# Kernel tuning notes

Measured on AMD Instinct MI355X. Metric: run time of the kernel, lower is better.

The kernel has to match this reference:

```python
import jax, jax.numpy as jnp
import numpy as np

B, C, H, W = 16, 1536, 32, 32
M = 64      # num_clusters
L = 128     # cluster_dim
G = 256     # token_dim
HID = 512
OT_ITERS = 3
EPS = 1e-6


def setup_inputs() -> dict:
    key = jax.random.key(0)
    ks = jax.random.split(key, 12)
    def w(k, shape, fan_in):
        return jax.random.normal(k, shape, jnp.float32) * (1.0 / np.sqrt(fan_in))
    return {
        'x': jax.random.normal(ks[0], (B, C, H, W), jnp.float32),
        't': jax.random.normal(ks[1], (B, C), jnp.float32),
        # token_features: Linear(C->512), ReLU, Linear(512->G)
        'Wt1': w(ks[2], (HID, C), C), 'bt1': jnp.zeros((HID,), jnp.float32),
        'Wt2': w(ks[3], (G, HID), HID), 'bt2': jnp.zeros((G,), jnp.float32),
        # cluster_features: 1x1 Conv(C->512), ReLU, 1x1 Conv(512->L)
        'Wc1': w(ks[4], (HID, C), C), 'bc1': jnp.zeros((HID,), jnp.float32),
        'Wc2': w(ks[5], (L, HID), HID), 'bc2': jnp.zeros((L,), jnp.float32),
        # score: 1x1 Conv(C->512), ReLU, 1x1 Conv(512->M)
        'Ws1': w(ks[6], (HID, C), C), 'bs1': jnp.zeros((HID,), jnp.float32),
        'Ws2': w(ks[7], (M, HID), HID), 'bs2': jnp.zeros((M,), jnp.float32),
        # temp_predictor: Conv1d(L->1, k=1)
        'Wtp': w(ks[8], (L,), L), 'btp': jnp.zeros((), jnp.float32),
        'dust_bin': jnp.asarray(1.0, jnp.float32),
        'burst_b': jnp.asarray(0.0, jnp.float32),
        'burst_p': jnp.asarray(1.0, jnp.float32),
        'lambda_discount': jnp.asarray(0.5, jnp.float32),
    }


def _log_optimal_transport(scores, alpha, iters):
    # scores: [B, m, n]; alpha: scalar dust-bin logit
    b, m, n = scores.shape
    Z0 = jnp.concatenate([scores, jnp.broadcast_to(alpha, (b, 1, n))], axis=1)  # [B, m+1, n]
    norm = -jnp.log(jnp.asarray(m + n, scores.dtype))
    log_mu = jnp.concatenate([jnp.full((m,), norm, scores.dtype),
                              (jnp.log(jnp.asarray(n, scores.dtype)) + norm)[None]])  # [m+1]
    log_nu = jnp.full((n,), norm, scores.dtype)
    u = jnp.zeros((b, m + 1), scores.dtype)
    v = jnp.zeros((b, n), scores.dtype)
    for _ in range(iters):
        u = log_mu - jax.nn.logsumexp(Z0 + v[:, None, :], axis=2)
        v = log_nu - jax.nn.logsumexp(Z0 + u[:, :, None], axis=1)
    return Z0 + u[:, :, None] + v[:, None, :] - norm


def _l2norm(a, axis):
    return a / jnp.maximum(jnp.linalg.norm(a, axis=axis, keepdims=True), 1e-12)


def _forward(x, t, Wt1, bt1, Wt2, bt2, Wc1, bc1, Wc2, bc2, Ws1, bs1, Ws2, bs2,
             Wtp, btp, dust_bin, burst_b, burst_p, lambda_discount):
    b, c, h, w = x.shape
    n = h * w
    xf = x.reshape(b, c, n)  # [B, C, N] (1x1 convs == per-pixel MLP)
    # cluster features f: [B, L, N]
    h1 = jax.nn.relu(jnp.einsum('bcn,oc->bon', xf, Wc1) + bc1[:, None])
    f = jnp.einsum('bhn,lh->bln', h1, Wc2) + bc2[:, None]
    # assignment scores p: [B, M, N]
    h2 = jax.nn.relu(jnp.einsum('bcn,oc->bon', xf, Ws1) + bs1[:, None])
    p = jnp.einsum('bhn,mh->bmn', h2, Ws2) + bs2[:, None]
    # global token: [B, G]
    tok = jax.nn.relu(t @ Wt1.T + bt1) @ Wt2.T + bt2
    # Sinkhorn OT soft assignment, drop dust bin row
    P = jnp.exp(_log_optimal_transport(p, dust_bin, OT_ITERS))[:, :-1, :]  # [B, M, N]
    # burst-aware weighting
    f_norm = _l2norm(f, axis=1)                                  # [B, L, N]
    T_i = jax.nn.softplus(jnp.einsum('bln,l->bn', f, Wtp) + btp)  # [B, N]
    sim = jnp.einsum('bli,blj->bij', f_norm, f_norm)              # [B, N, N]
    T_avg = (T_i[:, :, None] + T_i[:, None, :]) * 0.5
    burst_w = jax.nn.sigmoid(T_avg * sim + burst_b)
    discount = jnp.clip(jnp.sum(burst_w, axis=-1) ** burst_p, 1e-3, 1e3)  # [B, N]
    lam = jax.nn.sigmoid(lambda_discount)
    P_adj = (1.0 - lam) * P + lam * (P / (discount[:, None, :] + EPS))
    # local aggregation: (f[:, :, None, :] * P[:, None, :, :]).sum(-1) == batched matmul
    agg = jnp.einsum('bln,bmn->blm', f, P_adj)  # [B, L, M]
    agg = _l2norm(agg, axis=1).reshape(b, -1)   # [B, L*M]
    tok_n = _l2norm(tok, axis=-1)
    g = jnp.concatenate([tok_n, agg], axis=-1)  # [B, G + L*M]
    return _l2norm(g, axis=-1)


def reference(x, t, Wt1, bt1, Wt2, bt2, Wc1, bc1, Wc2, bc2, Ws1, bs1, Ws2, bs2,
              Wtp, btp, dust_bin, burst_b, burst_p, lambda_discount):
    return _forward(x, t, Wt1, bt1, Wt2, bt2, Wc1, bc1, Wc2, bc2, Ws1, bs1, Ws2, bs2,
                    Wtp, btp, dust_bin, burst_b, burst_p, lambda_discount)
```

## Files before the change

kernel.cpp:

```cpp
#include <hip/hip_runtime.h>
#include <math.h>

#define B_   16
#define C_   1536
#define N_   1024
#define M_   64
#define L_   128
#define G_   256
#define HID_ 512

typedef __attribute__((ext_vector_type(8))) short short8;
typedef __attribute__((ext_vector_type(4))) float floatx4;

__device__ __forceinline__ unsigned short f2bf_rne(float x) {
    unsigned u = __float_as_uint(x);
    unsigned r = u + 0x7fffu + ((u >> 16) & 1u);
    return (unsigned short)(r >> 16);
}
__device__ __forceinline__ unsigned pack_bf2(float lo, float hi) {
    unsigned a = __float_as_uint(lo) + 0x8000u;
    unsigned b = __float_as_uint(hi) + 0x8000u;
    return (a >> 16) | (b & 0xffff0000u);
}

__device__ __forceinline__ void gl2lds16(const void* g, void* l) {
    __builtin_amdgcn_global_load_lds(
        (const __attribute__((address_space(1))) void*)g,
        (__attribute__((address_space(3))) void*)l, 16, 0, 0);
}

__global__ __launch_bounds__(256) void cast_w_kernel(
    const float* __restrict__ Wc1, const float* __restrict__ Ws1,
    const float* __restrict__ Wc2, const float* __restrict__ Ws2,
    unsigned short* __restrict__ Wbf, unsigned short* __restrict__ W2)
{
    const int V1 = 393216;
    const int VH = 196608;
    int idx = blockIdx.x * 256 + threadIdx.x;
    if (idx < V1) {
        const float4* src = (idx < VH) ? (const float4*)Wc1 : (const float4*)Ws1;
        float4 v = src[(idx < VH) ? idx : idx - VH];
        ushort4 o;
        o.x = f2bf_rne(v.x); o.y = f2bf_rne(v.y);
        o.z = f2bf_rne(v.z); o.w = f2bf_rne(v.w);
        ((ushort4*)Wbf)[idx] = o;
    } else if (idx < V1 + 192 * 1024) {
        int i2 = idx - V1;
        int row = i2 >> 10, k = i2 & 1023;
        float v = 0.f;
        if (row < 128) { if (k < 512) v = Wc2[row * 512 + k]; }
        else           { if (k >= 512) v = Ws2[(row - 128) * 512 + (k - 512)]; }
        W2[i2] = f2bf_rne(v);
    }
}

__global__ __launch_bounds__(256) void xt_kernel(
    const float* __restrict__ x, unsigned short* __restrict__ xT)
{
    __shared__ float Xs[64][65];
    const int t = threadIdx.x;
    const int n0 = blockIdx.x * 64, c0 = blockIdx.y * 64, b = blockIdx.z;
    const float* xb = x + (long)b * C_ * N_;
    #pragma unroll
    for (int it = 0; it < 4; ++it) {
        int idx = it * 256 + t, cr = idx >> 4, fc = idx & 15;
        float4 v = *(const float4*)&xb[(long)(c0 + cr) * N_ + n0 + fc * 4];
        Xs[cr][fc * 4 + 0] = v.x;
        Xs[cr][fc * 4 + 1] = v.y;
        Xs[cr][fc * 4 + 2] = v.z;
        Xs[cr][fc * 4 + 3] = v.w;
    }
    __syncthreads();
    uint2* xo = (uint2*)(xT + (long)b * N_ * C_);
    #pragma unroll
    for (int it = 0; it < 4; ++it) {
        int idx = it * 256 + t, nr = idx >> 4, pc = idx & 15;
        uint2 o;
        o.x = pack_bf2(Xs[4 * pc + 0][nr], Xs[4 * pc + 1][nr]);
        o.y = pack_bf2(Xs[4 * pc + 2][nr], Xs[4 * pc + 3][nr]);
        xo[(long)(n0 + nr) * 384 + (c0 >> 2) + pc] = o;
    }
}

#define G1_STAGE_A(kt, q)                                                    \
    gl2lds16(aSrc + (long)(q) * (32 * C_) + (kt) * 64,                       \
             (char*)g1lds + (((kt) & 1) * 65536 + (q) * 8192) + sdst)
#define G1_STAGE_B(kt, q)                                                    \
    gl2lds16(bSrc + (long)(q) * (32 * C_) + (kt) * 64,                       \
             (char*)g1lds + (((kt) & 1) * 65536 + 32768 + (q) * 8192) + sdst)

#define G1_PHASE(q, STAGES, TAIL)                                            \
  {                                                                          \
    const char* ab = cb + aFB + (q) * 8192;                                  \
    short8 a0 = *(const short8*)(ab + ks0);                                  \
    short8 a1 = *(const short8*)(ab + ks1);                                  \
    short8 a2 = *(const short8*)(ab + 2048 + ks0);                           \
    short8 a3 = *(const short8*)(ab + 2048 + ks1);                           \
    STAGES                                                                   \
    __builtin_amdgcn_s_barrier();                                            \
    asm volatile("s_waitcnt lgkmcnt(0)" ::: "memory");                       \
    __builtin_amdgcn_sched_barrier(0);                                       \
    __builtin_amdgcn_s_setprio(1);                                           \
    _Pragma("unroll")                                                        \
    for (int fj = 0; fj < 4; ++fj) {                                         \
      acc[2*(q)][fj]   = __builtin_amdgcn_mfma_f32_16x16x32_bf16(            \
          a0, bfr[fj][0], acc[2*(q)][fj], 0, 0, 0);                          \
      acc[2*(q)][fj]   = __builtin_amdgcn_mfma_f32_16x16x32_bf16(            \
          a1, bfr[fj][1], acc[2*(q)][fj], 0, 0, 0);                          \
      acc[2*(q)+1][fj] = __builtin_amdgcn_mfma_f32_16x16x32_bf16(            \
          a2, bfr[fj][0], acc[2*(q)+1][fj], 0, 0, 0);                        \
      acc[2*(q)+1][fj] = __builtin_amdgcn_mfma_f32_16x16x32_bf16(            \
          a3, bfr[fj][1], acc[2*(q)+1][fj], 0, 0, 0);                        \
    }                                                                        \
    __builtin_amdgcn_s_setprio(0);                                           \
    TAIL                                                                     \
    __builtin_amdgcn_s_barrier();                                            \
    __builtin_amdgcn_sched_barrier(0);                                       \
  }

#define G1_TILE(tt, S1, S2, TAIL3)                                           \
  {                                                                          \
    const char* cb = (const char*)g1lds + ((tt) & 1) * 65536;                \
    _Pragma("unroll")                                                        \
    for (int fj = 0; fj < 4; ++fj) {                                         \
      const char* bb = cb + bFB + (fj >> 1) * 8192 + (fj & 1) * 2048;        \
      bfr[fj][0] = *(const short8*)(bb + ks0);                               \
      bfr[fj][1] = *(const short8*)(bb + ks1);                               \
    }                                                                        \
    G1_PHASE(0, if (S1) { G1_STAGE_A((tt)+1, 2); G1_STAGE_A((tt)+1, 3); }, ) \
    G1_PHASE(1, if (S2) { G1_STAGE_B((tt)+2, 0); G1_STAGE_B((tt)+2, 1); }, ) \
    G1_PHASE(2, if (S2) { G1_STAGE_B((tt)+2, 2); G1_STAGE_B((tt)+2, 3); }, ) \
    G1_PHASE(3, if (S2) { G1_STAGE_A((tt)+2, 0); G1_STAGE_A((tt)+2, 1); }, TAIL3) \
  }

__global__ __launch_bounds__(512, 2) void gemm1_kernel(
    const unsigned short* __restrict__ Wbf, const unsigned short* __restrict__ xT,
    const float* __restrict__ bc1, const float* __restrict__ bs1,
    unsigned short* __restrict__ hT)
{
    __shared__ unsigned short g1lds[65536];
    const int t = threadIdx.x;
    const int lane = t & 63, w = t >> 6;
    const int n0 = blockIdx.x * 256, o0 = blockIdx.y * 256, b = blockIdx.z;

    const int sgrow = ((t & 256) ? 128 : 0) + ((t >> 3) & 31);
    const int sdst  = t * 16;
    const int sslot = ((t & 7) ^ ((t >> 3) & 7)) * 8;
    const unsigned short* aSrc = Wbf + (long)(o0 + sgrow) * C_ + sslot;
    const unsigned short* bSrc = xT + (long)b * N_ * C_
                               + (long)(n0 + sgrow) * C_ + sslot;

    const int lrow = lane & 15, kgrp = lane >> 4;
    const int wo = (w >> 2) * 128, wn = (w & 3) * 64;
    const int aFB = (w >> 2) * 4096 + lrow * 128;
    const int bFB = 32768 + ((w >> 1) & 1) * 4096 + (w & 1) * 16384 + lrow * 128;
    const int ks0 = (kgrp ^ (lrow & 7)) * 16;
    const int ks1 = ((4 + kgrp) ^ (lrow & 7)) * 16;

    floatx4 acc[8][4];
    #pragma unroll
    for (int i = 0; i < 8; ++i)
        #pragma unroll
        for (int j = 0; j < 4; ++j) acc[i][j] = (floatx4)0.0f;
    short8 bfr[4][2];

    #pragma unroll
    for (int q = 0; q < 4; ++q) { G1_STAGE_A(0, q); G1_STAGE_B(0, q); }
    #pragma unroll
    for (int q = 0; q < 4; ++q) G1_STAGE_B(1, q);
    G1_STAGE_A(1, 0); G1_STAGE_A(1, 1);
    asm volatile("s_waitcnt vmcnt(6)" ::: "memory");
    __builtin_amdgcn_s_barrier();
    __builtin_amdgcn_sched_barrier(0);

    #pragma unroll 2
    for (int t8 = 0; t8 < 22; ++t8)
        G1_TILE(t8, 1, 1, asm volatile("s_waitcnt vmcnt(6)" ::: "memory");)
    G1_TILE(22, 1, 0, asm volatile("s_waitcnt vmcnt(0)" ::: "memory");)
    G1_TILE(23, 0, 0, )

    const float* bias = (o0 < 512) ? bc1 : bs1;
    const int ob = (o0 < 512) ? o0 : o0 - 512;
    #pragma unroll
    for (int fi = 0; fi < 8; ++fi) {
        const int orow = wo + fi * 16 + kgrp * 4;
        float4 bv = *(const float4*)&bias[ob + orow];
        #pragma unroll
        for (int fj = 0; fj < 4; ++fj) {
            const int n = n0 + wn + fj * 16 + lrow;
            float v0 = fmaxf(acc[fi][fj][0] + bv.x, 0.f);
            float v1 = fmaxf(acc[fi][fj][1] + bv.y, 0.f);
            float v2 = fmaxf(acc[fi][fj][2] + bv.z, 0.f);
            float v3 = fmaxf(acc[fi][fj][3] + bv.w, 0.f);
            uint2 pk;
            pk.x = ((unsigned)f2bf_rne(v0)) | (((unsigned)f2bf_rne(v1)) << 16);
            pk.y = ((unsigned)f2bf_rne(v2)) | (((unsigned)f2bf_rne(v3)) << 16);
            *(uint2*)&hT[((long)b * N_ + n) * 1024 + o0 + orow] = pk;
        }
    }
}

__global__ __launch_bounds__(256, 2) void gemm23_kernel(
    const unsigned short* __restrict__ W2, const unsigned short* __restrict__ hT,
    const float* __restrict__ bc2, const float* __restrict__ bs2,
    float* __restrict__ f, float* __restrict__ p)
{
    __shared__ unsigned short As[64 * 32];
    __shared__ unsigned short Bs[128 * 32];
    const int t = threadIdx.x;
    const int lane = t & 63, w = t >> 6;
    const int n0 = blockIdx.x * 128, o0 = blockIdx.y * 64, b = blockIdx.z;
    const unsigned short* hTb = hT + (long)b * N_ * 1024;

    const int wo = (w >> 1) * 32, wn = (w & 1) * 64;
    const int lrow = lane & 15, kgrp = lane >> 4;
    const int arow = t >> 2, acol = (t & 3) * 8;
    const int klo = (o0 < 128) ? 0 : 512;

    floatx4 acc[2][4];
    #pragma unroll
    for (int i = 0; i < 2; ++i)
        #pragma unroll
        for (int j = 0; j < 4; ++j) acc[i][j] = (floatx4)0.0f;

    for (int k0 = 0; k0 < 512; k0 += 32) {
        gl2lds16(W2 + (long)(o0 + arow) * 1024 + klo + k0 + acol, (char*)As + t * 16);
        #pragma unroll
        for (int r = 0; r < 2; ++r)
            gl2lds16(hTb + (long)(n0 + r * 64 + arow) * 1024 + klo + k0 + acol,
                     (char*)Bs + r * 4096 + t * 16);
        __syncthreads();
        short8 af[2], bfr[4];
        #pragma unroll
        for (int i = 0; i < 2; ++i)
            af[i] = *(const short8*)((const char*)As +
                        (wo + i * 16 + lrow) * 64 + kgrp * 16);
        #pragma unroll
        for (int j = 0; j < 4; ++j)
            bfr[j] = *(const short8*)((const char*)Bs +
                        (wn + j * 16 + lrow) * 64 + kgrp * 16);
        #pragma unroll
        for (int i = 0; i < 2; ++i)
            #pragma unroll
            for (int j = 0; j < 4; ++j)
                acc[i][j] = __builtin_amdgcn_mfma_f32_16x16x32_bf16(
                    af[i], bfr[j], acc[i][j], 0, 0, 0);
        __syncthreads();
    }

    #pragma unroll
    for (int i = 0; i < 2; ++i) {
        int o = o0 + wo + i * 16 + kgrp * 4;
        #pragma unroll
        for (int j = 0; j < 4; ++j) {
            int n = n0 + wn + j * 16 + lrow;
            #pragma unroll
            for (int r = 0; r < 4; ++r) {
                int oo = o + r;
                float v = acc[i][j][r];
                if (oo < 128) f[((long)b * L_ + oo) * N_ + n] = v + bc2[oo];
                else p[((long)b * M_ + (oo - 128)) * N_ + n] = v + bs2[oo - 128];
            }
        }
    }
}

__global__ __launch_bounds__(256) void token1_kernel(
    const float* __restrict__ t_in, const float* __restrict__ Wt1,
    const float* __restrict__ bt1, float* __restrict__ hid)
{
    const int lane = threadIdx.x & 63, w = threadIdx.x >> 6;
    const int o = blockIdx.x * 4 + w, b = blockIdx.y;
    const float4* wr = (const float4*)(Wt1 + (long)o * C_);
    const float4* tb = (const float4*)(t_in + (long)b * C_);
    float acc = 0.f;
    #pragma unroll
    for (int i = 0; i < 6; ++i) {
        float4 a = wr[i * 64 + lane], tv = tb[i * 64 + lane];
        acc += a.x * tv.x + a.y * tv.y + a.z * tv.z + a.w * tv.w;
    }
    #pragma unroll
    for (int off = 1; off < 64; off <<= 1) acc += __shfl_xor(acc, off);
    if (lane == 0) hid[b * HID_ + o] = fmaxf(acc + bt1[o], 0.f);
}

__global__ __launch_bounds__(256) void token2_kernel(
    const float* __restrict__ hid, const float* __restrict__ Wt2,
    const float* __restrict__ bt2, float* __restrict__ tok)
{
    const int lane = threadIdx.x & 63, w = threadIdx.x >> 6;
    const int g = blockIdx.x * 4 + w, b = blockIdx.y;
    const float4* wr = (const float4*)(Wt2 + (long)g * HID_);
    const float4* hb = (const float4*)(hid + (long)b * HID_);
    float acc = 0.f;
    #pragma unroll
    for (int i = 0; i < 2; ++i) {
        float4 a = wr[i * 64 + lane], hv = hb[i * 64 + lane];
        acc += a.x * hv.x + a.y * hv.y + a.z * hv.z + a.w * hv.w;
    }
    #pragma unroll
    for (int off = 1; off < 64; off <<= 1) acc += __shfl_xor(acc, off);
    if (lane == 0) tok[b * G_ + g] = acc + bt2[g];
}

__global__ __launch_bounds__(256) void token3_kernel(
    const float* __restrict__ tok, float* __restrict__ tokn)
{
    __shared__ float red[4];
    const int b = blockIdx.x, t = threadIdx.x;
    float v = tok[b * G_ + t];
    float ss = v * v;
    #pragma unroll
    for (int off = 1; off < 64; off <<= 1) ss += __shfl_xor(ss, off);
    if ((t & 63) == 0) red[t >> 6] = ss;
    __syncthreads();
    float inv = 1.f / fmaxf(sqrtf(red[0] + red[1] + red[2] + red[3]), 1e-12f);
    tokn[b * G_ + t] = v * inv;
}

__global__ __launch_bounds__(256) void ku_first_kernel(
    float* __restrict__ p, const float* __restrict__ dust,
    float* __restrict__ avec)
{
    const int t = threadIdx.x, lane = t & 63, w = t >> 6;
    const int m = blockIdx.x * 4 + w, b = blockIdx.y;
    if (m > M_) return;
    float s = 0.f;
    if (m < M_) {
        float* row = p + ((long)b * M_ + m) * N_;
        #pragma unroll
        for (int i = 0; i < 16; ++i) {
            int n = i * 64 + lane;
            float K = expf(row[n]);
            row[n] = K;
            s += K;
        }
    } else {
        s = 16.f * expf(dust[0]);
    }
    #pragma unroll
    for (int off = 1; off < 64; off <<= 1) s += __shfl_xor(s, off);
    if (lane == 0) {
        float mu = (m < M_) ? (1.f / 1088.f) : (1024.f / 1088.f);
        avec[b * (M_ + 1) + m] = mu / s;
    }
}

__global__ __launch_bounds__(256) void kvku_kernel(
    const float* __restrict__ K, const float* __restrict__ dust,
    const float* __restrict__ avec_in, float* __restrict__ avec_out)
{
    __shared__ float a_s[M_ + 1];
    __shared__ float b_lds[N_];
    const int t = threadIdx.x, lane = t & 63, w = t >> 6;
    const int mg = blockIdx.x, b = blockIdx.y;
    const float ea = expf(dust[0]);
    const float* Kb = K + (long)b * M_ * N_;

    if (t < M_ + 1) a_s[t] = avec_in[b * (M_ + 1) + t];
    __syncthreads();

    #pragma unroll
    for (int k = 0; k < 4; ++k) {
        int n = k * 256 + t;
        float s = ea * a_s[M_];
        const float* col = Kb + n;
        #pragma unroll
        for (int m = 0; m < M_; ++m) s = fmaf(col[(long)m * N_], a_s[m], s);
        b_lds[n] = (1.f / 1088.f) / s;
    }
    __syncthreads();

    const int m = mg * 4 + w;
    if (m > M_) return;
    float s = 0.f;
    if (m < M_) {
        const float* row = Kb + (long)m * N_;
        #pragma unroll
        for (int i = 0; i < 16; ++i) {
            int n = i * 64 + lane;
            s = fmaf(row[n], b_lds[n], s);
        }
    } else {
        #pragma unroll
        for (int i = 0; i < 16; ++i) s += b_lds[i * 64 + lane];
        s *= ea;
    }
    #pragma unroll
    for (int off = 1; off < 64; off <<= 1) s += __shfl_xor(s, off);
    if (lane == 0) {
        float mu = (m < M_) ? (1.f / 1088.f) : (1024.f / 1088.f);
        avec_out[b * (M_ + 1) + m] = mu / s;
    }
}

__global__ __launch_bounds__(256) void tnorm_kernel(
    const float* __restrict__ f, const float* __restrict__ Wtp,
    const float* __restrict__ btp, unsigned short* __restrict__ fnT,
    float* __restrict__ T, float* __restrict__ draw)
{
    __shared__ float Ft[L_][65];
    __shared__ float red_ss[4][64];
    __shared__ float red_dot[4][64];
    __shared__ float invs[64];
    __shared__ float wtp_s[L_];
    const int b = blockIdx.y, n0 = blockIdx.x * 64, t = threadIdx.x;
    const float* fb = f + (long)b * L_ * N_;

    if (t < L_) wtp_s[t] = Wtp[t];
    for (int it = 0; it < 32; ++it) {
        int idx = it * 256 + t;
        int l = idx >> 6, c = idx & 63;
        Ft[l][c] = fb[(long)l * N_ + n0 + c];
    }
    __syncthreads();
    {
        const int lg = t >> 6, col = t & 63;
        float ss = 0.f, dot = 0.f;
        #pragma unroll
        for (int i = 0; i < 32; ++i) {
            int l = lg * 32 + i;
            float v = Ft[l][col];
            ss = fmaf(v, v, ss);
            dot = fmaf(v, wtp_s[l], dot);
        }
        red_ss[lg][col] = ss;
        red_dot[lg][col] = dot;
    }
    __syncthreads();
    if (t < 64) {
        float ss = ((red_ss[0][t] + red_ss[1][t]) + (red_ss[2][t] + red_ss[3][t]));
        float dot = ((red_dot[0][t] + red_dot[1][t]) + (red_dot[2][t] + red_dot[3][t]));
        invs[t] = 1.f / fmaxf(sqrtf(ss), 1e-12f);
        float xx = dot + btp[0];
        T[b * N_ + n0 + t] = (xx > 0.f) ? (xx + log1pf(expf(-xx)))
                                        : log1pf(expf(xx));
        draw[b * N_ + n0 + t] = 0.f;
    }
    __syncthreads();
    unsigned* fo = (unsigned*)fnT;
    for (int it = 0; it < 16; ++it) {
        int idx = it * 256 + t;
        int nl = idx >> 6, jp = idx & 63;
        float inv = invs[nl];
        fo[(((long)b * N_ + n0 + nl) << 6) + jp] =
            pack_bf2(Ft[2 * jp][nl] * inv, Ft[2 * jp + 1][nl] * inv);
    }
}

__global__ __launch_bounds__(256) void sim_kernel(
    const unsigned short* __restrict__ fnT, const float* __restrict__ T,
    const float* __restrict__ bb, float* __restrict__ draw)
{
    __shared__ unsigned short As[64 * 136];
    __shared__ unsigned short Bs[64 * 136];
    __shared__ float Ti[64], Tj[64];
    const int b = blockIdx.z, i0 = blockIdx.y * 64, j0base = blockIdx.x * 256;
    const int t = threadIdx.x, lane = t & 63, w = t >> 6;
    const int lrow = lane & 15, kgrp = lane >> 4;
    const unsigned short* fb = fnT + (long)b * N_ * 128;
    const float burstb = bb[0];

    if (t < 64) Ti[t] = T[b * N_ + i0 + t];
    const int srow = t >> 4, scol = (t & 15) * 8;
    #pragma unroll
    for (int r = 0; r < 4; ++r) {
        uint4 av = *(const uint4*)(fb + (long)(i0 + r * 16 + srow) * 128 + scol);
        *(uint4*)((char*)As + (r * 16 + srow) * 272 + scol * 2) = av;
    }
    uint4 bv[4];
    #pragma unroll
    for (int r = 0; r < 4; ++r)
        bv[r] = *(const uint4*)(fb + (long)(j0base + r * 16 + srow) * 128 + scol);

    float rs[4] = {0.f, 0.f, 0.f, 0.f};
    #pragma unroll
    for (int jj = 0; jj < 4; ++jj) {
        __syncthreads();
        #pragma unroll
        for (int r = 0; r < 4; ++r)
            *(uint4*)((char*)Bs + (r * 16 + srow) * 272 + scol * 2) = bv[r];
        if (t >= 64 && t < 128) Tj[t - 64] = T[b * N_ + j0base + jj * 64 + (t - 64)];
        if (jj < 3) {
            #pragma unroll
            for (int r = 0; r < 4; ++r)
                bv[r] = *(const uint4*)(fb +
                    (long)(j0base + (jj + 1) * 64 + r * 16 + srow) * 128 + scol);
        }
        __syncthreads();

        floatx4 acc[4];
        #pragma unroll
        for (int j = 0; j < 4; ++j) acc[j] = (floatx4)0.0f;
        __builtin_amdgcn_s_setprio(1);
        #pragma unroll
        for (int k0 = 0; k0 < 128; k0 += 32) {
            short8 af = *(const short8*)((const char*)As +
                            (w * 16 + lrow) * 272 + k0 * 2 + kgrp * 16);
            #pragma unroll
            for (int j = 0; j < 4; ++j) {
                short8 bf = *(const short8*)((const char*)Bs +
                                (j * 16 + lrow) * 272 + k0 * 2 + kgrp * 16);
                acc[j] = __builtin_amdgcn_mfma_f32_16x16x32_bf16(af, bf, acc[j], 0, 0, 0);
            }
        }
        __builtin_amdgcn_s_setprio(0);
        #pragma unroll
        for (int j = 0; j < 4; ++j) {
            float Tjv = Tj[j * 16 + lrow];
            #pragma unroll
            for (int r = 0; r < 4; ++r) {
                float Tiv = Ti[w * 16 + kgrp * 4 + r];
                float xarg = 0.5f * (Tiv + Tjv) * acc[j][r] + burstb;
                rs[r] += 1.f / (1.f + expf(-xarg));
            }
        }
    }

    #pragma unroll
    for (int off = 1; off < 16; off <<= 1)
        #pragma unroll
        for (int r = 0; r < 4; ++r) rs[r] += __shfl_xor(rs[r], off);
    if (lrow == 0) {
        #pragma unroll
        for (int r = 0; r < 4; ++r)
            atomicAdd(&draw[b * N_ + i0 + w * 16 + kgrp * 4 + r], rs[r]);
    }
}

__global__ __launch_bounds__(256) void agg_kernel(
    const float* __restrict__ f, const float* __restrict__ Kmat,
    const float* __restrict__ avec, const float* __restrict__ dust,
    const float* __restrict__ draw, const float* __restrict__ bp,
    const float* __restrict__ lamd, float* __restrict__ aggp)
{
    __shared__ float fch[L_][65];
    __shared__ float Pch[M_][65];
    __shared__ float a_s[M_ + 1], cf[64];
    const int b = blockIdx.y, nb = blockIdx.x, n0 = nb * 64;
    const int t = threadIdx.x, tx = t & 15, ty = t >> 4;
    const float* fb = f + (long)b * L_ * N_;
    const float* Kb = Kmat + (long)b * M_ * N_;

    if (t < M_ + 1) a_s[t] = avec[b * (M_ + 1) + t];
    __syncthreads();

    for (int idx = t; idx < L_ * 64; idx += 256) {
        int l = idx >> 6, c = idx & 63;
        fch[l][c] = fb[(long)l * N_ + n0 + c];
    }
    for (int idx = t; idx < M_ * 64; idx += 256) {
        int m = idx >> 6, c = idx & 63;
        Pch[m][c] = Kb[(long)m * N_ + n0 + c] * a_s[m];
    }
    __syncthreads();

    if (t < 64) {
        float s = expf(dust[0]) * a_s[M_];
        #pragma unroll
        for (int m = 0; m < M_; ++m) s += Pch[m][t];
        float d = powf(draw[b * N_ + n0 + t], bp[0]);
        d = fminf(fmaxf(d, 1e-3f), 1e3f);
        float lam = 1.f / (1.f + expf(-lamd[0]));
        cf[t] = ((1.f - lam) + lam / (d + 1e-6f)) / s;
    }
    __syncthreads();

    float acc[8][4] = {};
    for (int n = 0; n < 64; ++n) {
        float cfn = cf[n];
        float fv[8], pv[4];
        #pragma unroll
        for (int i = 0; i < 8; ++i) fv[i] = fch[ty + 16 * i][n];
        #pragma unroll
        for (int j = 0; j < 4; ++j) pv[j] = Pch[tx * 4 + j][n] * cfn;
        #pragma unroll
        for (int i = 0; i < 8; ++i)
            #pragma unroll
            for (int j = 0; j < 4; ++j)
                acc[i][j] = fmaf(fv[i], pv[j], acc[i][j]);
    }
    float* op = aggp + ((long)b * 16 + nb) * (L_ * M_);
    #pragma unroll
    for (int i = 0; i < 8; ++i) {
        float4 v = make_float4(acc[i][0], acc[i][1], acc[i][2], acc[i][3]);
        *(float4*)&op[(ty + 16 * i) * M_ + tx * 4] = v;
    }
}

__global__ __launch_bounds__(256) void final_kernel(
    const float* __restrict__ tokn, const float* __restrict__ aggp,
    float* __restrict__ out)
{
    __shared__ float ar[L_ * M_];
    __shared__ float invm[M_];
    __shared__ float red[4];
    __shared__ float s_invtot;
    const int b = blockIdx.x, t = threadIdx.x;
    const float* pb = aggp + (long)b * 16 * (L_ * M_);

    for (int idx = t; idx < L_ * M_; idx += 256) {
        float s = 0.f;
        #pragma unroll
        for (int nb = 0; nb < 16; ++nb) s += pb[nb * (L_ * M_) + idx];
        ar[idx] = s;
    }
    __syncthreads();

    if (t < 64) {
        float ss = 0.f;
        for (int l = 0; l < L_; ++l) {
            float v = ar[l * M_ + t];
            ss = fmaf(v, v, ss);
        }
        invm[t] = 1.f / fmaxf(sqrtf(ss), 1e-12f);
    }
    __syncthreads();

    float part;
    {
        float tn = tokn[b * G_ + t];
        part = tn * tn;
    }
    for (int idx = t; idx < L_ * M_; idx += 256) {
        float v = ar[idx] * invm[idx & 63];
        part = fmaf(v, v, part);
    }
    for (int off = 32; off; off >>= 1) part += __shfl_down(part, off);
    if ((t & 63) == 0) red[t >> 6] = part;
    __syncthreads();
    if (t == 0)
        s_invtot = 1.f / fmaxf(sqrtf(red[0] + red[1] + red[2] + red[3]), 1e-12f);
    __syncthreads();

    const float invtot = s_invtot;
    float* ob = out + (long)b * (G_ + L_ * M_);
    ob[t] = tokn[b * G_ + t] * invtot;
    for (int idx = t; idx < L_ * M_; idx += 256)
        ob[G_ + idx] = ar[idx] * invm[idx & 63] * invtot;
}

extern "C" void kernel_launch(void* const* d_in, const int* in_sizes, int n_in,
                              void* d_out, int out_size, void* d_ws, size_t ws_size,
                              hipStream_t stream)
{
    const float* x    = (const float*)d_in[0];
    const float* t_in = (const float*)d_in[1];
    const float* Wt1  = (const float*)d_in[2];
    const float* bt1  = (const float*)d_in[3];
    const float* Wt2  = (const float*)d_in[4];
    const float* bt2  = (const float*)d_in[5];
    const float* Wc1  = (const float*)d_in[6];
    const float* bc1  = (const float*)d_in[7];
    const float* Wc2  = (const float*)d_in[8];
    const float* bc2  = (const float*)d_in[9];
    const float* Ws1  = (const float*)d_in[10];
    const float* bs1  = (const float*)d_in[11];
    const float* Ws2  = (const float*)d_in[12];
    const float* bs2  = (const float*)d_in[13];
    const float* Wtp  = (const float*)d_in[14];
    const float* btp  = (const float*)d_in[15];
    const float* dust = (const float*)d_in[16];
    const float* bb   = (const float*)d_in[17];
    const float* bp   = (const float*)d_in[18];
    const float* lamd = (const float*)d_in[19];

    char* wsb = (char*)d_ws;
    unsigned short* xT  = (unsigned short*)wsb;
    float* f    = (float*)(wsb + 0);
    float* p    = (float*)(wsb + 8388608);
    unsigned short* fnT = (unsigned short*)(wsb + 12582912);
    float* hid  = (float*)(wsb + 16777216);
    float* tok  = (float*)(wsb + 16809984);
    float* tokn = (float*)(wsb + 16826368);
    float* T    = (float*)(wsb + 16842752);
    float* draw = (float*)(wsb + 16908288);
    float* avec = (float*)(wsb + 17563648);
    float* avec2= (float*)(wsb + 17567808);
    unsigned short* hT  = (unsigned short*)(wsb + 50331648);
    unsigned short* Wbf = (unsigned short*)(wsb + 83886080);
    unsigned short* W2  = (unsigned short*)(wsb + 87031808);
    float* aggp = (float*)(wsb + 87425024);
    float* out  = (float*)d_out;

    cast_w_kernel<<<2304, 256, 0, stream>>>(Wc1, Ws1, Wc2, Ws2, Wbf, W2);

    xt_kernel   <<<dim3(16, 24, 16), 256, 0, stream>>>(x, xT);
    gemm1_kernel<<<dim3(4, 4, 16), 512, 0, stream>>>(Wbf, xT, bc1, bs1, hT);
    gemm23_kernel<<<dim3(8, 3, 16), 256, 0, stream>>>(W2, hT, bc2, bs2, f, p);

    token1_kernel<<<dim3(128, 16), 256, 0, stream>>>(t_in, Wt1, bt1, hid);
    token2_kernel<<<dim3(64, 16), 256, 0, stream>>>(hid, Wt2, bt2, tok);
    token3_kernel<<<16, 256, 0, stream>>>(tok, tokn);

    ku_first_kernel<<<dim3(17, 16), 256, 0, stream>>>(p, dust, avec);
    kvku_kernel    <<<dim3(17, 16), 256, 0, stream>>>(p, dust, avec, avec2);
    kvku_kernel    <<<dim3(17, 16), 256, 0, stream>>>(p, dust, avec2, avec);

    tnorm_kernel<<<dim3(16, 16), 256, 0, stream>>>(f, Wtp, btp, fnT, T, draw);
    sim_kernel  <<<dim3(4, 16, 16), 256, 0, stream>>>(fnT, T, bb, draw);
    agg_kernel  <<<dim3(16, 16), 256, 0, stream>>>(f, p, avec, dust, draw, bp, lamd, aggp);
    final_kernel<<<16, 256, 0, stream>>>(tokn, aggp, out);
}
```

Before: 371.2 us.

## Fuse Sinkhorn exp and row sums into GEMM epilogue; merge token MLP kernels

The score GEMM epilogue now applies exp to the logits, stores K, and writes per-block partial row sums. This removes the separate ku_first pass that re-read and rewrote the score matrix, and the first kvku iteration rebuilds the row scaling from those partials. The three token-MLP kernels become one kernel with one block per batch, keeping intermediates in LDS. That cuts launches but runs only 16 blocks, and each wave loops serially over many dot products, so the token path may become latency-bound.

```diff
diff --git a/kernel.cpp b/kernel.cpp
--- a/kernel.cpp
+++ b/kernel.cpp
@@ -203,10 +203,11 @@
 __global__ __launch_bounds__(256, 2) void gemm23_kernel(
     const unsigned short* __restrict__ W2, const unsigned short* __restrict__ hT,
     const float* __restrict__ bc2, const float* __restrict__ bs2,
-    float* __restrict__ f, float* __restrict__ p)
+    float* __restrict__ f, float* __restrict__ p, float* __restrict__ part)
 {
     __shared__ unsigned short As[64 * 32];
     __shared__ unsigned short Bs[128 * 32];
+    __shared__ float prs[M_][2];
     const int t = threadIdx.x;
     const int lane = t & 63, w = t >> 6;
     const int n0 = blockIdx.x * 128, o0 = blockIdx.y * 64, b = blockIdx.z;
@@ -248,67 +249,91 @@
         __syncthreads();
     }
 
-    #pragma unroll
-    for (int i = 0; i < 2; ++i) {
-        int o = o0 + wo + i * 16 + kgrp * 4;
-        #pragma unroll
-        for (int j = 0; j < 4; ++j) {
-            int n = n0 + wn + j * 16 + lrow;
+    if (o0 < 128) {
+        #pragma unroll
+        for (int i = 0; i < 2; ++i) {
+            int o = o0 + wo + i * 16 + kgrp * 4;
+            #pragma unroll
+            for (int j = 0; j < 4; ++j) {
+                int n = n0 + wn + j * 16 + lrow;
+                #pragma unroll
+                for (int r = 0; r < 4; ++r)
+                    f[((long)b * L_ + o + r) * N_ + n] = acc[i][j][r] + bc2[o + r];
+            }
+        }
+    } else {
+        float pir[2][4];
+        #pragma unroll
+        for (int i = 0; i < 2; ++i) {
+            const int m = wo + i * 16 + kgrp * 4;
+            #pragma unroll
+            for (int r = 0; r < 4; ++r) pir[i][r] = 0.f;
+            #pragma unroll
+            for (int j = 0; j < 4; ++j) {
+                int n = n0 + wn + j * 16 + lrow;
+                #pragma unroll
+                for (int r = 0; r < 4; ++r) {
+                    float K = expf(acc[i][j][r] + bs2[m + r]);
+                    p[((long)b * M_ + m + r) * N_ + n] = K;
+                    pir[i][r] += K;
+                }
+            }
             #pragma unroll
             for (int r = 0; r < 4; ++r) {
-                int oo = o + r;
-                float v = acc[i][j][r];
-                if (oo < 128) f[((long)b * L_ + oo) * N_ + n] = v + bc2[oo];
-                else p[((long)b * M_ + (oo - 128)) * N_ + n] = v + bs2[oo - 128];
+                float s = pir[i][r];
+                s += __shfl_xor(s, 1); s += __shfl_xor(s, 2);
+                s += __shfl_xor(s, 4); s += __shfl_xor(s, 8);
+                if (lrow == 0) prs[m + r][w & 1] = s;
             }
         }
-    }
-}
-
-__global__ __launch_bounds__(256) void token1_kernel(
+        __syncthreads();
+        if (t < M_)
+            part[((long)b * 8 + blockIdx.x) * M_ + t] = prs[t][0] + prs[t][1];
+    }
+}
+
+__global__ __launch_bounds__(256) void token_kernel(
     const float* __restrict__ t_in, const float* __restrict__ Wt1,
-    const float* __restrict__ bt1, float* __restrict__ hid)
-{
-    const int lane = threadIdx.x & 63, w = threadIdx.x >> 6;
-    const int o = blockIdx.x * 4 + w, b = blockIdx.y;
-    const float4* wr = (const float4*)(Wt1 + (long)o * C_);
-    const float4* tb = (const float4*)(t_in + (long)b * C_);
-    float acc = 0.f;
-    #pragma unroll
-    for (int i = 0; i < 6; ++i) {
-        float4 a = wr[i * 64 + lane], tv = tb[i * 64 + lane];
-        acc += a.x * tv.x + a.y * tv.y + a.z * tv.z + a.w * tv.w;
-    }
-    #pragma unroll
-    for (int off = 1; off < 64; off <<= 1) acc += __shfl_xor(acc, off);
-    if (lane == 0) hid[b * HID_ + o] = fmaxf(acc + bt1[o], 0.f);
-}
-
-__global__ __launch_bounds__(256) void token2_kernel(
-    const float* __restrict__ hid, const float* __restrict__ Wt2,
-    const float* __restrict__ bt2, float* __restrict__ tok)
-{
-    const int lane = threadIdx.x & 63, w = threadIdx.x >> 6;
-    const int g = blockIdx.x * 4 + w, b = blockIdx.y;
-    const float4* wr = (const float4*)(Wt2 + (long)g * HID_);
-    const float4* hb = (const float4*)(hid + (long)b * HID_);
-    float acc = 0.f;
-    #pragma unroll
-    for (int i = 0; i < 2; ++i) {
-        float4 a = wr[i * 64 + lane], hv = hb[i * 64 + lane];
-        acc += a.x * hv.x + a.y * hv.y + a.z * hv.z + a.w * hv.w;
-    }
-    #pragma unroll
-    for (int off = 1; off < 64; off <<= 1) acc += __shfl_xor(acc, off);
-    if (lane == 0) tok[b * G_ + g] = acc + bt2[g];
-}
-
-__global__ __launch_bounds__(256) void token3_kernel(
-    const float* __restrict__ tok, float* __restrict__ tokn)
-{
+    const float* __restrict__ bt1, const float* __restrict__ Wt2,
+    const float* __restrict__ bt2, float* __restrict__ tokn)
+{
+    __shared__ __align__(16) float hid_s[HID_];
+    __shared__ __align__(16) float tok_s[G_];
     __shared__ float red[4];
     const int b = blockIdx.x, t = threadIdx.x;
-    float v = tok[b * G_ + t];
+    const int lane = t & 63, w = t >> 6;
+    const float4* tb = (const float4*)(t_in + (long)b * C_);
+
+    for (int rep = 0; rep < 128; ++rep) {
+        const int o = w * 128 + rep;
+        const float4* wr = (const float4*)(Wt1 + (long)o * C_);
+        float acc = 0.f;
+        #pragma unroll
+        for (int i = 0; i < 6; ++i) {
+            float4 a = wr[i * 64 + lane], tv = tb[i * 64 + lane];
+            acc += a.x * tv.x + a.y * tv.y + a.z * tv.z + a.w * tv.w;
+        }
+        #pragma unroll
+        for (int off = 1; off < 64; off <<= 1) acc += __shfl_xor(acc, off);
+        if (lane == 0) hid_s[o] = fmaxf(acc + bt1[o], 0.f);
+    }
+    __syncthreads();
+    const float4* hb = (const float4*)hid_s;
+    for (int rep = 0; rep < 64; ++rep) {
+        const int g = w * 64 + rep;
+        const float4* wr = (const float4*)(Wt2 + (long)g * HID_);
+        float acc = 0.f;
+        #pragma unroll
+        for (int i = 0; i < 2; ++i) {
+            float4 a = wr[i * 64 + lane], hv = hb[i * 64 + lane];
+            acc += a.x * hv.x + a.y * hv.y + a.z * hv.z + a.w * hv.w;
+        }
+        #pragma unroll
+        for (int off = 1; off < 64; off <<= 1) acc += __shfl_xor(acc, off);
+        if (lane == 0) tok_s[g] = acc + bt2[g];
+    }
+    __syncthreads();
+    float v = tok_s[t];
     float ss = v * v;
     #pragma unroll
     for (int off = 1; off < 64; off <<= 1) ss += __shfl_xor(ss, off);
@@ -318,37 +343,10 @@
     tokn[b * G_ + t] = v * inv;
 }
 
-__global__ __launch_bounds__(256) void ku_first_kernel(
-    float* __restrict__ p, const float* __restrict__ dust,
-    float* __restrict__ avec)
-{
-    const int t = threadIdx.x, lane = t & 63, w = t >> 6;
-    const int m = blockIdx.x * 4 + w, b = blockIdx.y;
-    if (m > M_) return;
-    float s = 0.f;
-    if (m < M_) {
-        float* row = p + ((long)b * M_ + m) * N_;
-        #pragma unroll
-        for (int i = 0; i < 16; ++i) {
-            int n = i * 64 + lane;
-            float K = expf(row[n]);
-            row[n] = K;
-            s += K;
-        }
-    } else {
-        s = 16.f * expf(dust[0]);
-    }
-    #pragma unroll
-    for (int off = 1; off < 64; off <<= 1) s += __shfl_xor(s, off);
-    if (lane == 0) {
-        float mu = (m < M_) ? (1.f / 1088.f) : (1024.f / 1088.f);
-        avec[b * (M_ + 1) + m] = mu / s;
-    }
-}
-
+template<bool FIRST>
 __global__ __launch_bounds__(256) void kvku_kernel(
     const float* __restrict__ K, const float* __restrict__ dust,
-    const float* __restrict__ avec_in, float* __restrict__ avec_out)
+    const float* __restrict__ ain, float* __restrict__ avec_out)
 {
     __shared__ float a_s[M_ + 1];
     __shared__ float b_lds[N_];
@@ -357,7 +355,18 @@
     const float ea = expf(dust[0]);
     const float* Kb = K + (long)b * M_ * N_;
 
-    if (t < M_ + 1) a_s[t] = avec_in[b * (M_ + 1) + t];
+    if (FIRST) {
+        if (t < M_) {
+            float s = 0.f;
+            #pragma unroll
+            for (int nx = 0; nx < 8; ++nx) s += ain[((long)b * 8 + nx) * M_ + t];
+            a_s[t] = (1.f / 1088.f) / s;
+        } else if (t == M_) {
+            a_s[M_] = (1024.f / 1088.f) / (1024.f * ea);
+        }
+    } else {
+        if (t < M_ + 1) a_s[t] = ain[b * (M_ + 1) + t];
+    }
     __syncthreads();
 
     #pragma unroll
@@ -670,11 +679,10 @@
     float* f    = (float*)(wsb + 0);
     float* p    = (float*)(wsb + 8388608);
     unsigned short* fnT = (unsigned short*)(wsb + 12582912);
-    float* hid  = (float*)(wsb + 16777216);
-    float* tok  = (float*)(wsb + 16809984);
     float* tokn = (float*)(wsb + 16826368);
     float* T    = (float*)(wsb + 16842752);
     float* draw = (float*)(wsb + 16908288);
+    float* part = (float*)(wsb + 16973824);
     float* avec = (float*)(wsb + 17563648);
     float* avec2= (float*)(wsb + 17567808);
     unsigned short* hT  = (unsigned short*)(wsb + 50331648);
@@ -687,15 +695,12 @@
 
     xt_kernel   <<<dim3(16, 24, 16), 256, 0, stream>>>(x, xT);
     gemm1_kernel<<<dim3(4, 4, 16), 512, 0, stream>>>(Wbf, xT, bc1, bs1, hT);
-    gemm23_kernel<<<dim3(8, 3, 16), 256, 0, stream>>>(W2, hT, bc2, bs2, f, p);
-
-    token1_kernel<<<dim3(128, 16), 256, 0, stream>>>(t_in, Wt1, bt1, hid);
-    token2_kernel<<<dim3(64, 16), 256, 0, stream>>>(hid, Wt2, bt2, tok);
-    token3_kernel<<<16, 256, 0, stream>>>(tok, tokn);
-
-    ku_first_kernel<<<dim3(17, 16), 256, 0, stream>>>(p, dust, avec);
-    kvku_kernel    <<<dim3(17, 16), 256, 0, stream>>>(p, dust, avec, avec2);
-    kvku_kernel    <<<dim3(17, 16), 256, 0, stream>>>(p, dust, avec2, avec);
+    gemm23_kernel<<<dim3(8, 3, 16), 256, 0, stream>>>(W2, hT, bc2, bs2, f, p, part);
+
+    token_kernel<<<16, 256, 0, stream>>>(t_in, Wt1, bt1, Wt2, bt2, tokn);
+
+    kvku_kernel<true> <<<dim3(17, 16), 256, 0, stream>>>(p, dust, part, avec2);
+    kvku_kernel<false><<<dim3(17, 16), 256, 0, stream>>>(p, dust, avec2, avec);
 
     tnorm_kernel<<<dim3(16, 16), 256, 0, stream>>>(f, Wtp, btp, fnT, T, draw);
     sim_kernel  <<<dim3(4, 16, 16), 256, 0, stream>>>(fnT, T, bb, draw);
```

After: 570.2 us. +53.6%, slower.
